# Kernel optimization log

Hardware: AMD Instinct MI355X
Metric: run time of the kernel (lower is better)

The kernel has to match this reference:

```python
import jax, jax.numpy as jnp
import numpy as np

N = 1_000_000          # points
C_IN = 10              # decorated point features
C_OUT = 64             # pillar feature channels
S = 30_000             # number of pillars (segments)
EPS = 1e-3             # BatchNorm1d eps


def setup_inputs() -> dict:
    key = jax.random.key(0)
    ks = jax.random.split(key, 8)
    inputs = jax.random.normal(ks[0], (N, C_IN), dtype=jnp.float32)
    # every pillar gets ~N/S points; sorted, all segments non-empty
    unq_inv = jnp.sort(jnp.arange(N, dtype=jnp.int32) % S)
    W_lin = jax.random.normal(ks[1], (C_OUT, C_IN), dtype=jnp.float32) * 0.3
    gamma = 1.0 + 0.1 * jax.random.normal(ks[2], (C_OUT,), dtype=jnp.float32)
    beta = 0.1 * jax.random.normal(ks[3], (C_OUT,), dtype=jnp.float32)
    dw1 = jax.random.normal(ks[4], (C_OUT,), dtype=jnp.float32) * 0.5      # depthwise 1x1 conv (groups=C)
    pw1 = jax.random.normal(ks[5], (C_OUT, C_OUT), dtype=jnp.float32) * 0.1  # pointwise 1x1 conv
    dw2 = jax.random.normal(ks[6], (C_OUT,), dtype=jnp.float32) * 0.5
    pw2 = jax.random.normal(ks[7], (C_OUT, C_OUT), dtype=jnp.float32) * 0.1
    return {"inputs": inputs, "unq_inv": unq_inv, "W_lin": W_lin,
            "gamma": gamma, "beta": beta, "dw1": dw1, "pw1": pw1,
            "dw2": dw2, "pw2": pw2}


def reference(inputs, unq_inv, W_lin, gamma, beta, dw1, pw1, dw2, pw2):
    # Linear (no bias) -> BN (training-mode batch stats) -> ReLU
    x = inputs @ W_lin.T                                   # [N, C]
    mu = jnp.mean(x, axis=0)
    var = jnp.mean(jnp.square(x - mu), axis=0)             # biased var, as torch BN
    x = (x - mu) * jax.lax.rsqrt(var + EPS) * gamma + beta
    x = jax.nn.relu(x)

    # MAFF attention: local branch (depthwise scale -> swish -> 1x1 conv)
    s = x * dw1                                            # groups=C 1x1 conv == per-channel scale
    xl = (s * jax.nn.sigmoid(s)) @ pw1.T                   # [N, C]
    # global branch: avg-pool over points -> depthwise scale -> relu -> 1x1 conv
    g = jnp.mean(x, axis=0)                                # [C]
    xg = pw2 @ jax.nn.relu(dw2 * g)                        # [C]
    wei = jax.nn.sigmoid(xl + xg)                          # broadcast [N,C] + [C]
    xi = x * (1.0 + wei)

    # segment reductions keyed by pillar id (scatter_max + scatter_sum)
    x_max = jax.ops.segment_max(xi, unq_inv, num_segments=S,
                                indices_are_sorted=True)
    x_sum = jax.ops.segment_sum(xi, unq_inv, num_segments=S,
                                indices_are_sorted=True)
    return x_max + x_sum                                   # [S, C]
```

## Files before the change

kernel.cpp:

```cpp
#include <hip/hip_runtime.h>
#include <math.h>

#define N_PTS   1000000
#define CI      10
#define C       64
#define NSEG    30000
#define BN_EPS  1e-3f
#define FROFF   31104


using f32x4 = __attribute__((ext_vector_type(4))) float;
using s16x8 = __attribute__((ext_vector_type(8))) short;

__device__ inline short f2bf(float x) {
    unsigned u = __float_as_uint(x);
    unsigned r = (u + 0x7fffu + ((u >> 16) & 1u)) >> 16;
    return (short)r;
}
__device__ inline unsigned pack_trunc(float lo, float hi) {
    return (__float_as_uint(hi) & 0xffff0000u) | (__float_as_uint(lo) >> 16);
}
__device__ inline float frcp(float x) { return __builtin_amdgcn_rcpf(x); }
__device__ inline void lds_fence() {
    asm volatile("s_waitcnt lgkmcnt(0)" ::: "memory");
}

__global__ void __launch_bounds__(256) k_moments(const float* __restrict__ inp,
                                                 const int* __restrict__ idx,
                                                 float* __restrict__ ws,
                                                 int* __restrict__ starts) {
    const int tid = threadIdx.x;
    float v[65];
#pragma unroll
    for (int k = 0; k < 65; ++k) v[k] = 0.f;

    for (int p = blockIdx.x * blockDim.x + tid; p < N_PTS; p += gridDim.x * blockDim.x) {
        const float2* r2 = (const float2*)(inp + (size_t)p * CI);
        float2 a0 = r2[0], a1 = r2[1], a2 = r2[2], a3 = r2[3], a4 = r2[4];
        float r[CI] = {a0.x, a0.y, a1.x, a1.y, a2.x, a2.y, a3.x, a3.y, a4.x, a4.y};
#pragma unroll
        for (int i = 0; i < CI; ++i) v[i] += r[i];
        int kk = 10;
#pragma unroll
        for (int i = 0; i < CI; ++i)
#pragma unroll
            for (int j = i; j < CI; ++j) { v[kk] = fmaf(r[i], r[j], v[kk]); ++kk; }

        int iv = idx[p];
        if (p == 0) starts[0] = 0;
        else if (idx[p - 1] != iv) starts[iv] = p;
    }

#pragma unroll
    for (int k = 0; k < 65; ++k) {
#pragma unroll
        for (int off = 32; off >= 1; off >>= 1)
            v[k] += __shfl_xor(v[k], off, 64);
    }
    __shared__ float red[4 * 65];
    const int wv = tid >> 6, ln = tid & 63;
    if (ln == 0) {
#pragma unroll
        for (int k = 0; k < 65; ++k) red[wv * 65 + k] = v[k];
    }
    __syncthreads();
    if (tid < 65)
        atomicAdd(&ws[tid], red[tid] + red[65 + tid] + red[130 + tid] + red[195 + tid]);
}

__global__ void __launch_bounds__(256) k_gstats(const float* __restrict__ inp,
                                                const float* __restrict__ W,
                                                const float* __restrict__ gamma,
                                                const float* __restrict__ beta,
                                                float* __restrict__ ws) {
    const int tid  = threadIdx.x;
    const int wv   = tid >> 6;
    const int lane = tid & 63;
    const int m = lane & 15;
    const int q = lane >> 4;

    __shared__ float wp[C * CI];
    __shared__ float bsh[C];

    if (tid < C) {
        const int c = tid;
        float w[CI];
#pragma unroll
        for (int i = 0; i < CI; ++i) w[i] = W[c * CI + i];
        const float inv_n = 1.f / (float)N_PTS;

        float mu = 0.f;
#pragma unroll
        for (int i = 0; i < CI; ++i) mu = fmaf(w[i], ws[i], mu);
        mu *= inv_n;

        float ex2 = 0.f;
        int kk = 10;
#pragma unroll
        for (int i = 0; i < CI; ++i)
#pragma unroll
            for (int j = i; j < CI; ++j) {
                float mm = ws[kk];
                float t = w[i] * w[j] * mm;
                ex2 += (i == j) ? t : 2.f * t;
                ++kk;
            }
        ex2 *= inv_n;

        float var = ex2 - mu * mu;
        float rstd = rsqrtf(var + BN_EPS);
        float a = rstd * gamma[c];
        float b = beta[c] - mu * a;
        bsh[c] = b;
#pragma unroll
        for (int i = 0; i < CI; ++i) wp[c * CI + i] = a * w[i];
    }
    __syncthreads();

    s16x8 wfr[4];
#pragma unroll
    for (int nt = 0; nt < 4; ++nt) {
        s16x8 t;
#pragma unroll
        for (int j = 0; j < 8; ++j) {
            int k = 8 * q + j;
            t[j] = (k < CI) ? f2bf(wp[(nt * 16 + m) * CI + k]) : (short)0;
        }
        wfr[nt] = t;
    }
    float bb[4];
#pragma unroll
    for (int nt = 0; nt < 4; ++nt) bb[nt] = bsh[nt * 16 + m];

    const int wid = blockIdx.x * 4 + wv;
    const int nw  = gridDim.x * 4;
    const int NB  = N_PTS / 16;

    float2 P0, P1, P2, P3;
    auto loadrows = [&](int pb) {
        const float* row = inp + (size_t)(pb + m) * CI;
        if (q == 0) {
            P0 = *(const float2*)(row);     P1 = *(const float2*)(row + 2);
            P2 = *(const float2*)(row + 4); P3 = *(const float2*)(row + 6);
        } else if (q == 1) {
            P0 = *(const float2*)(row + 8);
        }
    };
    P0 = P1 = P2 = P3 = make_float2(0.f, 0.f);

    float sm[4] = {0.f, 0.f, 0.f, 0.f};
    const f32x4 zero = {0.f, 0.f, 0.f, 0.f};

    if (wid < NB) loadrows(wid * 16);
    for (int b = wid; b < NB; b += nw) {
        float2 L0 = P0, L1 = P1, L2 = P2, L3 = P3;
        if (b + nw < NB) loadrows((b + nw) * 16);

        union { s16x8 v; unsigned u[4]; } t;
        t.v = s16x8{0, 0, 0, 0, 0, 0, 0, 0};
        if (q < 2) t.u[0] = pack_trunc(L0.x, L0.y);
        if (q == 0) {
            t.u[1] = pack_trunc(L1.x, L1.y);
            t.u[2] = pack_trunc(L2.x, L2.y);
            t.u[3] = pack_trunc(L3.x, L3.y);
        }

        f32x4 xt[4];
#pragma unroll
        for (int nt = 0; nt < 4; ++nt) {
            xt[nt] = __builtin_amdgcn_mfma_f32_16x16x32_bf16(t.v, wfr[nt], zero, 0, 0, 0);
#pragma unroll
            for (int r = 0; r < 4; ++r)
                sm[nt] += fmaxf(xt[nt][r] + bb[nt], 0.f);
        }
    }

#pragma unroll
    for (int nt = 0; nt < 4; ++nt) {
        sm[nt] += __shfl_xor(sm[nt], 16, 64);
        sm[nt] += __shfl_xor(sm[nt], 32, 64);
    }
    float S = sm[0];
    if (q == 1) S = sm[1];
    if (q == 2) S = sm[2];
    if (q == 3) S = sm[3];

    __shared__ float red[4 * 64];
    red[wv * 64 + lane] = S;
    __syncthreads();
    if (tid < 64)
        atomicAdd(&ws[256 + tid], red[tid] + red[64 + tid] + red[128 + tid] + red[192 + tid]);
}

__global__ void k_prep(const float* __restrict__ W,
                       const float* __restrict__ gamma,
                       const float* __restrict__ beta,
                       const float* __restrict__ dw1,
                       const float* __restrict__ pw1,
                       const float* __restrict__ dw2,
                       const float* __restrict__ pw2,
                       float* __restrict__ ws) {
    const int lane = threadIdx.x;
    const int m = lane & 15, q = lane >> 4;
    const float inv_n = 1.f / (float)N_PTS;

    __shared__ float WP[C * CI];
    __shared__ float BSH[C], T[C], XG[C];

    {
        float w[CI];
#pragma unroll
        for (int i = 0; i < CI; ++i) w[i] = W[lane * CI + i];
        float mu = 0.f;
#pragma unroll
        for (int i = 0; i < CI; ++i) mu = fmaf(w[i], ws[i], mu);
        mu *= inv_n;
        float ex2 = 0.f;
        int kk = 10;
#pragma unroll
        for (int i = 0; i < CI; ++i)
#pragma unroll
            for (int j = i; j < CI; ++j) {
                float mm = ws[kk];
                float t = w[i] * w[j] * mm;
                ex2 += (i == j) ? t : 2.f * t;
                ++kk;
            }
        ex2 *= inv_n;
        float var = ex2 - mu * mu;
        float rstd = rsqrtf(var + BN_EPS);
        float a = rstd * gamma[lane];
        BSH[lane] = beta[lane] - mu * a;
#pragma unroll
        for (int i = 0; i < CI; ++i) WP[lane * CI + i] = a * w[i];
        T[lane] = fmaxf(dw2[lane] * (ws[256 + lane] * inv_n), 0.f);
    }
    __syncthreads();

    {
        float acc = 0.f;
#pragma unroll
        for (int k = 0; k < C; ++k) acc = fmaf(pw2[lane * C + k], T[k], acc);
        XG[lane] = acc;
    }
    __syncthreads();

    float4* FR = (float4*)(ws + FROFF);
    union { float4 f; s16x8 v; } u;

#pragma unroll
    for (int nt = 0; nt < 4; ++nt) {
        s16x8 tt;
#pragma unroll
        for (int j = 0; j < 8; ++j) {
            int k = 8 * q + j;
            tt[j] = (k < CI) ? f2bf(WP[(nt * 16 + m) * CI + k]) : (short)0;
        }
        u.v = tt; FR[nt * 64 + lane] = u.f;
    }
#pragma unroll
    for (int nt = 0; nt < 4; ++nt)
#pragma unroll
        for (int kc = 0; kc < 2; ++kc) {
            const float* src = pw1 + (nt * 16 + m) * C + kc * 32 + q * 8;
            float4 p0 = *(const float4*)src, p1 = *(const float4*)(src + 4);
            s16x8 tt;
            tt[0] = f2bf(p0.x); tt[1] = f2bf(p0.y); tt[2] = f2bf(p0.z); tt[3] = f2bf(p0.w);
            tt[4] = f2bf(p1.x); tt[5] = f2bf(p1.y); tt[6] = f2bf(p1.z); tt[7] = f2bf(p1.w);
            u.v = tt; FR[(4 + nt * 2 + kc) * 64 + lane] = u.f;
        }
    float4 f;
    f.x = BSH[m]; f.y = BSH[16 + m]; f.z = BSH[32 + m]; f.w = BSH[48 + m];
    FR[12 * 64 + lane] = f;
    f.x = dw1[m]; f.y = dw1[16 + m]; f.z = dw1[32 + m]; f.w = dw1[48 + m];
    FR[13 * 64 + lane] = f;
    f.x = XG[m]; f.y = XG[16 + m]; f.z = XG[32 + m]; f.w = XG[48 + m];
    FR[14 * 64 + lane] = f;
}

#define LD 68
#define SEGW 2
struct Rows { float2 r0, r1, r2, r3; };
__global__ void __launch_bounds__(128) k_main(const float* __restrict__ inp,
                                              const float* __restrict__ ws,
                                              const int* __restrict__ starts,
                                              float* __restrict__ out) {
    const int tid  = threadIdx.x;
    const int wv   = tid >> 6;
    const int lane = tid & 63;
    const int m = lane & 15;
    const int q = lane >> 4;
    const f32x4 zero = {0.f, 0.f, 0.f, 0.f};

    const float4* FR = (const float4*)(ws + FROFF);
    union { float4 f; s16x8 v; } u;
    s16x8 wfr[4];
#pragma unroll
    for (int nt = 0; nt < 4; ++nt) { u.f = FR[nt * 64 + lane]; wfr[nt] = u.v; }
    s16x8 bfr[4][2];
#pragma unroll
    for (int nt = 0; nt < 4; ++nt)
#pragma unroll
        for (int kc = 0; kc < 2; ++kc) { u.f = FR[(4 + nt * 2 + kc) * 64 + lane]; bfr[nt][kc] = u.v; }
    const float4 bb4  = FR[12 * 64 + lane];
    const float4 d14  = FR[13 * 64 + lane];
    const float4 xg4  = FR[14 * 64 + lane];
    const float bb[4]  = {bb4.x, bb4.y, bb4.z, bb4.w};
    const float d1v[4] = {d14.x, d14.y, d14.z, d14.w};
    const float xgv[4] = {xg4.x, xg4.y, xg4.z, xg4.w};

    __shared__ float sb[2][16 * LD];
    float* my = sb[wv];

    const int w  = blockIdx.x * 2 + wv;
    const int s0 = w * SEGW;

    int st1 = starts[s0 + 1];
    int st2 = (s0 + 2 < NSEG) ? starts[s0 + 2] : N_PTS;
    const int start   = starts[s0];
    const int end_all = st2;

    int cur = s0;
    int end_cur = st1;

    float sm[4]  = {0.f, 0.f, 0.f, 0.f};
    float mxv[4] = {-INFINITY, -INFINITY, -INFINITY, -INFINITY};

    auto flushseg = [&](int s) {
#pragma unroll
        for (int nt = 0; nt < 4; ++nt) {
            sm[nt] += __shfl_xor(sm[nt], 16, 64);
            sm[nt] += __shfl_xor(sm[nt], 32, 64);
            mxv[nt] = fmaxf(mxv[nt], __shfl_xor(mxv[nt], 16, 64));
            mxv[nt] = fmaxf(mxv[nt], __shfl_xor(mxv[nt], 32, 64));
        }
        float S = sm[0], M = mxv[0];
        if (q == 1) { S = sm[1]; M = mxv[1]; }
        if (q == 2) { S = sm[2]; M = mxv[2]; }
        if (q == 3) { S = sm[3]; M = mxv[3]; }
        out[(size_t)s * C + lane] = S + M;
#pragma unroll
        for (int nt = 0; nt < 4; ++nt) { sm[nt] = 0.f; mxv[nt] = -INFINITY; }
    };

    auto loadrows = [&](int pb) -> Rows {
        Rows R;
        R.r0 = R.r1 = R.r2 = R.r3 = make_float2(0.f, 0.f);
        const float* row = inp + (size_t)min(pb + m, N_PTS - 1) * CI;
        if (q == 0) {
            R.r0 = *(const float2*)(row);     R.r1 = *(const float2*)(row + 2);
            R.r2 = *(const float2*)(row + 4); R.r3 = *(const float2*)(row + 6);
        } else if (q == 1) {
            R.r0 = *(const float2*)(row + 8);
        }
        return R;
    };

    Rows A = loadrows(start);
    Rows B = (start + 16 < end_all) ? loadrows(start + 16) : A;

    for (int base = start; base < end_all; base += 16) {
        Rows L = A;
        A = B;
        if (base + 32 < end_all) B = loadrows(base + 32);

        const int nb = min(16, end_all - base);

        union { s16x8 v; unsigned u[4]; } t;
        t.v = s16x8{0, 0, 0, 0, 0, 0, 0, 0};
        if (q < 2) t.u[0] = pack_trunc(L.r0.x, L.r0.y);
        if (q == 0) {
            t.u[1] = pack_trunc(L.r1.x, L.r1.y);
            t.u[2] = pack_trunc(L.r2.x, L.r2.y);
            t.u[3] = pack_trunc(L.r3.x, L.r3.y);
        }

        f32x4 xt[4];
#pragma unroll
        for (int nt = 0; nt < 4; ++nt)
            xt[nt] = __builtin_amdgcn_mfma_f32_16x16x32_bf16(t.v, wfr[nt], zero, 0, 0, 0);

        float xn[4][4];
#pragma unroll
        for (int nt = 0; nt < 4; ++nt)
#pragma unroll
            for (int r = 0; r < 4; ++r) {
                float x = fmaxf(xt[nt][r] + bb[nt], 0.f);
                xn[nt][r] = x;
                float sg = x * d1v[nt];
                float sw = sg * frcp(1.f + __expf(-sg));
                my[(4 * q + r) * LD + nt * 16 + m] = sw;
            }
        lds_fence();

        s16x8 av[2];
#pragma unroll
        for (int kc = 0; kc < 2; ++kc) {
            const float* src = &my[m * LD + kc * 32 + q * 8];
            float4 p0 = *(const float4*)src;
            float4 p1 = *(const float4*)(src + 4);
            union { s16x8 v; unsigned u[4]; } tt;
            tt.u[0] = pack_trunc(p0.x, p0.y);
            tt.u[1] = pack_trunc(p0.z, p0.w);
            tt.u[2] = pack_trunc(p1.x, p1.y);
            tt.u[3] = pack_trunc(p1.z, p1.w);
            av[kc] = tt.v;
        }

        f32x4 xi[4];
#pragma unroll
        for (int nt = 0; nt < 4; ++nt) {
            xi[nt] = __builtin_amdgcn_mfma_f32_16x16x32_bf16(av[0], bfr[nt][0], zero, 0, 0, 0);
            xi[nt] = __builtin_amdgcn_mfma_f32_16x16x32_bf16(av[1], bfr[nt][1], xi[nt], 0, 0, 0);
        }
        lds_fence();

#pragma unroll
        for (int nt = 0; nt < 4; ++nt)
#pragma unroll
            for (int r = 0; r < 4; ++r) {
                float v   = xi[nt][r] + xgv[nt];
                float wei = frcp(1.f + __expf(-v));
                float x   = xn[nt][r];
                xi[nt][r] = fmaf(x, wei, x);
            }

        const int fin = base + nb;
        if (fin <= end_cur) {
            if (nb == 16) {
#pragma unroll
                for (int nt = 0; nt < 4; ++nt)
#pragma unroll
                    for (int r = 0; r < 4; ++r) {
                        sm[nt] += xi[nt][r];
                        mxv[nt] = fmaxf(mxv[nt], xi[nt][r]);
                    }
            } else {
#pragma unroll
                for (int nt = 0; nt < 4; ++nt)
#pragma unroll
                    for (int r = 0; r < 4; ++r) {
                        bool act = (4 * q + r) < nb;
                        sm[nt] += act ? xi[nt][r] : 0.f;
                        mxv[nt] = fmaxf(mxv[nt], act ? xi[nt][r] : -INFINITY);
                    }
            }
            if (fin == end_cur) { flushseg(cur); ++cur; end_cur = st2; }
        } else {
            const int B = end_cur - base;
#pragma unroll
            for (int nt = 0; nt < 4; ++nt)
#pragma unroll
                for (int r = 0; r < 4; ++r) {
                    bool act = (4 * q + r) < B;
                    sm[nt] += act ? xi[nt][r] : 0.f;
                    mxv[nt] = fmaxf(mxv[nt], act ? xi[nt][r] : -INFINITY);
                }
            flushseg(cur); ++cur;
#pragma unroll
            for (int nt = 0; nt < 4; ++nt)
#pragma unroll
                for (int r = 0; r < 4; ++r) {
                    int pt = 4 * q + r;
                    bool act = (pt >= B) && (pt < nb);
                    sm[nt] += act ? xi[nt][r] : 0.f;
                    mxv[nt] = fmaxf(mxv[nt], act ? xi[nt][r] : -INFINITY);
                }
            end_cur = st2;
        }
    }
}

extern "C" void kernel_launch(void* const* d_in, const int* in_sizes, int n_in,
                              void* d_out, int out_size, void* d_ws, size_t ws_size,
                              hipStream_t stream) {
    const float* inp   = (const float*)d_in[0];
    const int*   unq   = (const int*)d_in[1];
    const float* W     = (const float*)d_in[2];
    const float* gamma = (const float*)d_in[3];
    const float* beta  = (const float*)d_in[4];
    const float* dw1   = (const float*)d_in[5];
    const float* pw1   = (const float*)d_in[6];
    const float* dw2   = (const float*)d_in[7];
    const float* pw2   = (const float*)d_in[8];
    float* out = (float*)d_out;
    float* ws  = (float*)d_ws;
    int* starts = (int*)ws + 1024;

    hipMemsetAsync(ws, 0, 384 * sizeof(float), stream);

    k_moments <<<1024, 256, 0, stream>>>(inp, unq, ws, starts);
    k_gstats  <<<1024, 256, 0, stream>>>(inp, W, gamma, beta, ws);
    k_prep    <<<1,    64,  0, stream>>>(W, gamma, beta, dw1, pw1, dw2, pw2, ws);
    k_main    <<<7500, 128, 0, stream>>>(inp, ws, starts, out);
}
```

Baseline: 269.3 us.

## Deepen load prefetch, process two tiles per iteration, and spread atomic accumulators

k_moments now prefetches the next point's features and segment ids one iteration ahead. k_gstats keeps two loads in flight instead of one. k_main handles two 16-row tiles per loop iteration with double-buffered LDS tiles and a four-deep row prefetch, so MFMA work on the two tiles can interleave and there are fewer LDS fences per point. The atomic accumulators in the workspace are strided apart to reduce same-address contention, which means a larger memset. In exchange, register pressure in k_main goes up and occupancy may drop.

```diff
diff --git a/kernel.cpp b/kernel.cpp
--- a/kernel.cpp
+++ b/kernel.cpp
@@ -8,6 +8,9 @@
 #define BN_EPS  1e-3f
 #define FROFF   31104
 
+#define MSTR 7
+#define GOFF 512
+#define GSTR 8
 
 using f32x4 = __attribute__((ext_vector_type(4))) float;
 using s16x8 = __attribute__((ext_vector_type(8))) short;
@@ -24,20 +27,34 @@
 __device__ inline void lds_fence() {
     asm volatile("s_waitcnt lgkmcnt(0)" ::: "memory");
 }
+
+struct Rows { float2 r0, r1, r2, r3; };
 
 __global__ void __launch_bounds__(256) k_moments(const float* __restrict__ inp,
                                                  const int* __restrict__ idx,
                                                  float* __restrict__ ws,
                                                  int* __restrict__ starts) {
     const int tid = threadIdx.x;
+    const int stride = gridDim.x * blockDim.x;
     float v[65];
 #pragma unroll
     for (int k = 0; k < 65; ++k) v[k] = 0.f;
 
-    for (int p = blockIdx.x * blockDim.x + tid; p < N_PTS; p += gridDim.x * blockDim.x) {
-        const float2* r2 = (const float2*)(inp + (size_t)p * CI);
-        float2 a0 = r2[0], a1 = r2[1], a2 = r2[2], a3 = r2[3], a4 = r2[4];
+    int p = blockIdx.x * blockDim.x + tid;
+    float2 a0, a1, a2, a3, a4;
+    int ic = 0, ip = 0;
+    auto ld = [&](int qq) {
+        const float2* r2 = (const float2*)(inp + (size_t)qq * CI);
+        a0 = r2[0]; a1 = r2[1]; a2 = r2[2]; a3 = r2[3]; a4 = r2[4];
+        ic = idx[qq]; ip = (qq > 0) ? idx[qq - 1] : ic;
+    };
+    if (p < N_PTS) ld(p);
+    while (p < N_PTS) {
         float r[CI] = {a0.x, a0.y, a1.x, a1.y, a2.x, a2.y, a3.x, a3.y, a4.x, a4.y};
+        const int cc = ic, cp = ip, cq = p;
+        const int pn = p + stride;
+        if (pn < N_PTS) ld(pn);
+
 #pragma unroll
         for (int i = 0; i < CI; ++i) v[i] += r[i];
         int kk = 10;
@@ -46,9 +63,9 @@
 #pragma unroll
             for (int j = i; j < CI; ++j) { v[kk] = fmaf(r[i], r[j], v[kk]); ++kk; }
 
-        int iv = idx[p];
-        if (p == 0) starts[0] = 0;
-        else if (idx[p - 1] != iv) starts[iv] = p;
+        if (cq == 0) starts[0] = 0;
+        else if (cp != cc) starts[cc] = cq;
+        p = pn;
     }
 
 #pragma unroll
@@ -65,7 +82,8 @@
     }
     __syncthreads();
     if (tid < 65)
-        atomicAdd(&ws[tid], red[tid] + red[65 + tid] + red[130 + tid] + red[195 + tid]);
+        atomicAdd(&ws[MSTR * tid],
+                  red[tid] + red[65 + tid] + red[130 + tid] + red[195 + tid]);
 }
 
 __global__ void __launch_bounds__(256) k_gstats(const float* __restrict__ inp,
@@ -91,7 +109,7 @@
 
         float mu = 0.f;
 #pragma unroll
-        for (int i = 0; i < CI; ++i) mu = fmaf(w[i], ws[i], mu);
+        for (int i = 0; i < CI; ++i) mu = fmaf(w[i], ws[MSTR * i], mu);
         mu *= inv_n;
 
         float ex2 = 0.f;
@@ -100,7 +118,7 @@
         for (int i = 0; i < CI; ++i)
 #pragma unroll
             for (int j = i; j < CI; ++j) {
-                float mm = ws[kk];
+                float mm = ws[MSTR * kk];
                 float t = w[i] * w[j] * mm;
                 ex2 += (i == j) ? t : 2.f * t;
                 ++kk;
@@ -136,42 +154,43 @@
     const int nw  = gridDim.x * 4;
     const int NB  = N_PTS / 16;
 
-    float2 P0, P1, P2, P3;
-    auto loadrows = [&](int pb) {
+    auto loadrows = [&](int pb) -> Rows {
+        Rows R;
+        R.r0 = R.r1 = R.r2 = R.r3 = make_float2(0.f, 0.f);
         const float* row = inp + (size_t)(pb + m) * CI;
         if (q == 0) {
-            P0 = *(const float2*)(row);     P1 = *(const float2*)(row + 2);
-            P2 = *(const float2*)(row + 4); P3 = *(const float2*)(row + 6);
+            R.r0 = *(const float2*)(row);     R.r1 = *(const float2*)(row + 2);
+            R.r2 = *(const float2*)(row + 4); R.r3 = *(const float2*)(row + 6);
         } else if (q == 1) {
-            P0 = *(const float2*)(row + 8);
-        }
-    };
-    P0 = P1 = P2 = P3 = make_float2(0.f, 0.f);
+            R.r0 = *(const float2*)(row + 8);
+        }
+        return R;
+    };
 
     float sm[4] = {0.f, 0.f, 0.f, 0.f};
     const f32x4 zero = {0.f, 0.f, 0.f, 0.f};
 
-    if (wid < NB) loadrows(wid * 16);
+    Rows A  = loadrows(wid * 16);
+    Rows Bv = loadrows((wid + nw) * 16);
     for (int b = wid; b < NB; b += nw) {
-        float2 L0 = P0, L1 = P1, L2 = P2, L3 = P3;
-        if (b + nw < NB) loadrows((b + nw) * 16);
+        Rows L = A; A = Bv;
+        if (b + 2 * nw < NB) Bv = loadrows((b + 2 * nw) * 16);
 
         union { s16x8 v; unsigned u[4]; } t;
         t.v = s16x8{0, 0, 0, 0, 0, 0, 0, 0};
-        if (q < 2) t.u[0] = pack_trunc(L0.x, L0.y);
+        if (q < 2) t.u[0] = pack_trunc(L.r0.x, L.r0.y);
         if (q == 0) {
-            t.u[1] = pack_trunc(L1.x, L1.y);
-            t.u[2] = pack_trunc(L2.x, L2.y);
-            t.u[3] = pack_trunc(L3.x, L3.y);
-        }
-
-        f32x4 xt[4];
+            t.u[1] = pack_trunc(L.r1.x, L.r1.y);
+            t.u[2] = pack_trunc(L.r2.x, L.r2.y);
+            t.u[3] = pack_trunc(L.r3.x, L.r3.y);
+        }
+
 #pragma unroll
         for (int nt = 0; nt < 4; ++nt) {
-            xt[nt] = __builtin_amdgcn_mfma_f32_16x16x32_bf16(t.v, wfr[nt], zero, 0, 0, 0);
+            f32x4 xt = __builtin_amdgcn_mfma_f32_16x16x32_bf16(t.v, wfr[nt], zero, 0, 0, 0);
 #pragma unroll
             for (int r = 0; r < 4; ++r)
-                sm[nt] += fmaxf(xt[nt][r] + bb[nt], 0.f);
+                sm[nt] += fmaxf(xt[r] + bb[nt], 0.f);
         }
     }
 
@@ -189,7 +208,8 @@
     red[wv * 64 + lane] = S;
     __syncthreads();
     if (tid < 64)
-        atomicAdd(&ws[256 + tid], red[tid] + red[64 + tid] + red[128 + tid] + red[192 + tid]);
+        atomicAdd(&ws[GOFF + GSTR * tid],
+                  red[tid] + red[64 + tid] + red[128 + tid] + red[192 + tid]);
 }
 
 __global__ void k_prep(const float* __restrict__ W,
@@ -213,7 +233,7 @@
         for (int i = 0; i < CI; ++i) w[i] = W[lane * CI + i];
         float mu = 0.f;
 #pragma unroll
-        for (int i = 0; i < CI; ++i) mu = fmaf(w[i], ws[i], mu);
+        for (int i = 0; i < CI; ++i) mu = fmaf(w[i], ws[MSTR * i], mu);
         mu *= inv_n;
         float ex2 = 0.f;
         int kk = 10;
@@ -221,7 +241,7 @@
         for (int i = 0; i < CI; ++i)
 #pragma unroll
             for (int j = i; j < CI; ++j) {
-                float mm = ws[kk];
+                float mm = ws[MSTR * kk];
                 float t = w[i] * w[j] * mm;
                 ex2 += (i == j) ? t : 2.f * t;
                 ++kk;
@@ -233,7 +253,7 @@
         BSH[lane] = beta[lane] - mu * a;
 #pragma unroll
         for (int i = 0; i < CI; ++i) WP[lane * CI + i] = a * w[i];
-        T[lane] = fmaxf(dw2[lane] * (ws[256 + lane] * inv_n), 0.f);
+        T[lane] = fmaxf(dw2[lane] * (ws[GOFF + GSTR * lane] * inv_n), 0.f);
     }
     __syncthreads();
 
@@ -280,7 +300,6 @@
 
 #define LD 68
 #define SEGW 2
-struct Rows { float2 r0, r1, r2, r3; };
 __global__ void __launch_bounds__(128) k_main(const float* __restrict__ inp,
                                               const float* __restrict__ ws,
                                               const int* __restrict__ starts,
@@ -309,8 +328,9 @@
     const float d1v[4] = {d14.x, d14.y, d14.z, d14.w};
     const float xgv[4] = {xg4.x, xg4.y, xg4.z, xg4.w};
 
-    __shared__ float sb[2][16 * LD];
-    float* my = sb[wv];
+    __shared__ float sb[2][2][16 * LD];
+    float* t0 = sb[wv][0];
+    float* t1 = sb[wv][1];
 
     const int w  = blockIdx.x * 2 + wv;
     const int s0 = w * SEGW;
@@ -356,67 +376,53 @@
         return R;
     };
 
-    Rows A = loadrows(start);
-    Rows B = (start + 16 < end_all) ? loadrows(start + 16) : A;
-
-    for (int base = start; base < end_all; base += 16) {
-        Rows L = A;
-        A = B;
-        if (base + 32 < end_all) B = loadrows(base + 32);
-
-        const int nb = min(16, end_all - base);
-
-        union { s16x8 v; unsigned u[4]; } t;
+    Rows A0 = loadrows(start);
+    Rows A1 = (start + 16 < end_all) ? loadrows(start + 16) : A0;
+    Rows B0 = (start + 32 < end_all) ? loadrows(start + 32) : A0;
+    Rows B1 = (start + 48 < end_all) ? loadrows(start + 48) : A0;
+
+    auto stage1 = [&](const Rows& L, float* __restrict__ tile, float (&xn)[4][4]) {
+        union { s16x8 v; unsigned uu[4]; } t;
         t.v = s16x8{0, 0, 0, 0, 0, 0, 0, 0};
-        if (q < 2) t.u[0] = pack_trunc(L.r0.x, L.r0.y);
+        if (q < 2) t.uu[0] = pack_trunc(L.r0.x, L.r0.y);
         if (q == 0) {
-            t.u[1] = pack_trunc(L.r1.x, L.r1.y);
-            t.u[2] = pack_trunc(L.r2.x, L.r2.y);
-            t.u[3] = pack_trunc(L.r3.x, L.r3.y);
-        }
-
-        f32x4 xt[4];
-#pragma unroll
-        for (int nt = 0; nt < 4; ++nt)
-            xt[nt] = __builtin_amdgcn_mfma_f32_16x16x32_bf16(t.v, wfr[nt], zero, 0, 0, 0);
-
-        float xn[4][4];
-#pragma unroll
-        for (int nt = 0; nt < 4; ++nt)
+            t.uu[1] = pack_trunc(L.r1.x, L.r1.y);
+            t.uu[2] = pack_trunc(L.r2.x, L.r2.y);
+            t.uu[3] = pack_trunc(L.r3.x, L.r3.y);
+        }
+#pragma unroll
+        for (int nt = 0; nt < 4; ++nt) {
+            f32x4 xt = __builtin_amdgcn_mfma_f32_16x16x32_bf16(t.v, wfr[nt], zero, 0, 0, 0);
 #pragma unroll
             for (int r = 0; r < 4; ++r) {
-                float x = fmaxf(xt[nt][r] + bb[nt], 0.f);
+                float x = fmaxf(xt[r] + bb[nt], 0.f);
                 xn[nt][r] = x;
                 float sg = x * d1v[nt];
                 float sw = sg * frcp(1.f + __expf(-sg));
-                my[(4 * q + r) * LD + nt * 16 + m] = sw;
+                tile[(4 * q + r) * LD + nt * 16 + m] = sw;
             }
-        lds_fence();
-
+        }
+    };
+
+    auto stage2 = [&](const float* __restrict__ tile, const float (&xn)[4][4],
+                      f32x4 (&xi)[4]) {
         s16x8 av[2];
 #pragma unroll
         for (int kc = 0; kc < 2; ++kc) {
-            const float* src = &my[m * LD + kc * 32 + q * 8];
+            const float* src = &tile[m * LD + kc * 32 + q * 8];
             float4 p0 = *(const float4*)src;
             float4 p1 = *(const float4*)(src + 4);
-            union { s16x8 v; unsigned u[4]; } tt;
-            tt.u[0] = pack_trunc(p0.x, p0.y);
-            tt.u[1] = pack_trunc(p0.z, p0.w);
-            tt.u[2] = pack_trunc(p1.x, p1.y);
-            tt.u[3] = pack_trunc(p1.z, p1.w);
+            union { s16x8 v; unsigned uu[4]; } tt;
+            tt.uu[0] = pack_trunc(p0.x, p0.y);
+            tt.uu[1] = pack_trunc(p0.z, p0.w);
+            tt.uu[2] = pack_trunc(p1.x, p1.y);
+            tt.uu[3] = pack_trunc(p1.z, p1.w);
             av[kc] = tt.v;
         }
-
-        f32x4 xi[4];
 #pragma unroll
         for (int nt = 0; nt < 4; ++nt) {
             xi[nt] = __builtin_amdgcn_mfma_f32_16x16x32_bf16(av[0], bfr[nt][0], zero, 0, 0, 0);
             xi[nt] = __builtin_amdgcn_mfma_f32_16x16x32_bf16(av[1], bfr[nt][1], xi[nt], 0, 0, 0);
-        }
-        lds_fence();
-
-#pragma unroll
-        for (int nt = 0; nt < 4; ++nt)
 #pragma unroll
             for (int r = 0; r < 4; ++r) {
                 float v   = xi[nt][r] + xgv[nt];
@@ -424,8 +430,12 @@
                 float x   = xn[nt][r];
                 xi[nt][r] = fmaf(x, wei, x);
             }
-
-        const int fin = base + nb;
+        }
+    };
+
+    auto accum = [&](const f32x4 (&xi)[4], int b16) {
+        const int nb = min(16, end_all - b16);
+        const int fin = b16 + nb;
         if (fin <= end_cur) {
             if (nb == 16) {
 #pragma unroll
@@ -447,7 +457,7 @@
             }
             if (fin == end_cur) { flushseg(cur); ++cur; end_cur = st2; }
         } else {
-            const int B = end_cur - base;
+            const int B = end_cur - b16;
 #pragma unroll
             for (int nt = 0; nt < 4; ++nt)
 #pragma unroll
@@ -468,6 +478,28 @@
                 }
             end_cur = st2;
         }
+    };
+
+    for (int base = start; base < end_all; base += 32) {
+        Rows L0 = A0, L1 = A1;
+        A0 = B0; A1 = B1;
+        if (base + 64 < end_all) B0 = loadrows(base + 64);
+        if (base + 80 < end_all) B1 = loadrows(base + 80);
+        const bool two = (base + 16) < end_all;
+
+        float xn0[4][4], xn1[4][4];
+        f32x4 xi0[4], xi1[4];
+
+        stage1(L0, t0, xn0);
+        if (two) stage1(L1, t1, xn1);
+        lds_fence();
+
+        stage2(t0, xn0, xi0);
+        if (two) stage2(t1, xn1, xi1);
+
+        accum(xi0, base);
+        if (two) accum(xi1, base + 16);
+        lds_fence();
     }
 }
 
@@ -487,7 +519,7 @@
     float* ws  = (float*)d_ws;
     int* starts = (int*)ws + 1024;
 
-    hipMemsetAsync(ws, 0, 384 * sizeof(float), stream);
+    hipMemsetAsync(ws, 0, 1024 * sizeof(float), stream);
 
     k_moments <<<1024, 256, 0, stream>>>(inp, unq, ws, starts);
     k_gstats  <<<1024, 256, 0, stream>>>(inp, W, gamma, beta, ws);
```

Measured after the change: 271.8 us. Within noise of the previous version (+0.9%).
